# Performance work log

Measured on AMD Instinct MI355X. Metric: run time of the kernel, lower is better.

## Reference

```python
import jax, jax.numpy as jnp
import numpy as np
import math

H = 512       # hidden_dim
NL = 4        # num_layers
N2 = 32       # d_state // 2
B, L = 8, 4096
DT_MIN, DT_MAX = 1e-3, 1e-1
EPS = 1e-5


def _layer_norm(x, gamma, beta):
    mu = jnp.mean(x, axis=-1, keepdims=True)
    var = jnp.mean(jnp.square(x - mu), axis=-1, keepdims=True)
    return (x - mu) * jax.lax.rsqrt(var + EPS) * gamma + beta


def setup_inputs() -> dict:
    key = jax.random.key(0)
    ks = jax.random.split(key, 8)
    x = jax.random.normal(ks[0], (B, L, H), dtype=jnp.float32)
    # S4DKernel buffers / params, stacked over layers
    log_dt = jax.random.uniform(ks[1], (NL, H)) * (math.log(DT_MAX) - math.log(DT_MIN)) + math.log(DT_MIN)
    A_imag = jnp.broadcast_to(math.pi * jnp.arange(N2, dtype=jnp.float32), (NL, H, N2)).copy()
    log_A_real = jnp.full((NL, H, N2), math.log(0.5), dtype=jnp.float32)
    C = jax.random.normal(ks[2], (NL, H, N2, 2), dtype=jnp.float32)  # view_as_real of cfloat
    D = jax.random.normal(ks[3], (NL, H), dtype=jnp.float32)
    # 1x1 Conv1d h -> 2h (pointwise linear over channels)
    W = jax.random.normal(ks[4], (NL, 2 * H, H), dtype=jnp.float32) / math.sqrt(H)
    b = jax.random.normal(ks[5], (NL, 2 * H), dtype=jnp.float32) * 0.01
    gamma = jnp.ones((NL, H), dtype=jnp.float32)
    beta = jnp.zeros((NL, H), dtype=jnp.float32)
    return dict(x=x, log_dt=log_dt, A_imag=A_imag, log_A_real=log_A_real,
                C=C, D=D, W=W, b=b, gamma=gamma, beta=beta)


def reference(x, log_dt, A_imag, log_A_real, C, D, W, b, gamma, beta):
    Bsz, Lseq, h = x.shape
    t = jnp.arange(Lseq, dtype=jnp.float32)
    for i in range(NL):
        # --- S4D kernel generation ---
        dt = jnp.exp(log_dt[i])                                    # (h,)
        Cc = C[i, ..., 0] + 1j * C[i, ..., 1]                      # (h, n)
        A = -jnp.exp(log_A_real[i]) + 1j * A_imag[i]               # (h, n)
        dA = A * dt[:, None]                                       # (h, n)
        Cmod = Cc * (jnp.exp(dA) - 1.0) / A                        # (h, n)
        # Vandermonde: exp(dA * l), reduced over state dim
        K = 2.0 * jnp.einsum('hn,hnl->hl', Cmod,
                             jnp.exp(dA[:, :, None] * t)).real     # (h, L)
        # --- FFT long convolution ---
        u = jnp.transpose(x, (0, 2, 1))                            # (B, h, L)
        kf = jnp.fft.rfft(K, n=2 * Lseq)                           # (h, L+1)
        uf = jnp.fft.rfft(u, n=2 * Lseq)                           # (B, h, L+1)
        y = jnp.fft.irfft(uf * kf, n=2 * Lseq)[..., :Lseq]         # (B, h, L)
        y = y + u * D[i][:, None]
        y = jax.nn.gelu(y, approximate=False)                      # torch nn.GELU default (erf)
        # 1x1 conv h -> 2h then GLU over channel dim
        z = jnp.einsum('oh,bhl->bol', W[i], y) + b[i][None, :, None]
        a, g = jnp.split(z, 2, axis=1)
        y = a * jax.nn.sigmoid(g)                                  # (B, h, L)
        y = jnp.transpose(y, (0, 2, 1))                            # (B, L, h)
        x = _layer_norm(y + x, gamma[i], beta[i])
    return x
```

## Files before the change

kernel.cpp:

```cpp
#include <hip/hip_runtime.h>
#include <hip/hip_bf16.h>
#include <math.h>

#define H 512
#define NL 4
#define N2 32
#define Bsz 8
#define Lseq 4096
#define BT (Bsz*Lseq)
#define LC2 64
#define NCC (BT/LC2)
#define CPB (Lseq/LC2)

typedef __attribute__((ext_vector_type(8))) short short8;
typedef __attribute__((ext_vector_type(4))) float float4v;


__device__ __forceinline__ float bf2f(unsigned short u) {
    union { unsigned int i; float f; } x; x.i = ((unsigned int)u) << 16; return x.f;
}
__device__ __forceinline__ unsigned short f2bf(float f) {
    union { float f; unsigned int i; } x; x.f = f;
    unsigned int u = x.i + 0x7fff + ((x.i >> 16) & 1);
    return (unsigned short)(u >> 16);
}
__device__ __forceinline__ uint2 pack4bf(float a, float b, float c, float d) {
    uint2 r;
    r.x = (unsigned)f2bf(a) | ((unsigned)f2bf(b) << 16);
    r.y = (unsigned)f2bf(c) | ((unsigned)f2bf(d) << 16);
    return r;
}
__device__ __forceinline__ void async_copy16(const void* g, void* l) {
    __builtin_amdgcn_global_load_lds(
        (const __attribute__((address_space(1))) void*)g,
        (__attribute__((address_space(3))) void*)l, 16, 0, 0);
}

__global__ void wconv_kernel(const float* __restrict__ W, unsigned short* __restrict__ Wbf) {
    int tid = blockIdx.x * 256 + threadIdx.x;
    Wbf[tid] = f2bf(W[tid]);
}

__global__ void params_kernel(const float* __restrict__ log_dt, const float* __restrict__ A_imag,
                              const float* __restrict__ log_A_real, const float* __restrict__ Cin,
                              float* __restrict__ dA, float* __restrict__ Ct) {
    int tid = blockIdx.x * 256 + threadIdx.x;
    int h = tid % H;
    int n = (tid / H) % N2;
    int layer = tid / (H * N2);
    float dt = expf(log_dt[layer * H + h]);
    int pidx = (layer * H + h) * N2 + n;
    float Are = -expf(log_A_real[pidx]);
    float Aim = A_imag[pidx];
    float dre = Are * dt, dim = Aim * dt;
    float er = expf(dre);
    float lre = er * cosf(dim), lim = er * sinf(dim);
    float nre = lre - 1.0f, nim = lim;
    float inv = 1.0f / (Are * Are + Aim * Aim);
    float tre = (nre * Are + nim * Aim) * inv;
    float tim = (nim * Are - nre * Aim) * inv;
    float Ccre = Cin[pidx * 2], Ccim = Cin[pidx * 2 + 1];
    int oidx = ((layer * N2 + n) * 2) * H + h;
    dA[oidx] = dre;  dA[oidx + H] = dim;
    Ct[oidx] = 2.0f * (Ccre * tre - Ccim * tim);
    Ct[oidx + H] = 2.0f * (Ccre * tim + Ccim * tre);
}

__global__ void kergen_k_kernel(const float* __restrict__ dA, const float* __restrict__ Ct,
                                unsigned short* __restrict__ kmat) {
    int t = blockIdx.x * 256 + threadIdx.x;
    int d = t & 63;
    int h = (t >> 6) & (H - 1);
    int layer = t >> 15;
    float fd = (float)d;
    float sum = 0.f;
    for (int n = 0; n < N2; n++) {
        int base = ((layer * N2 + n) * 2) * H + h;
        float dre = dA[base], dim = dA[base + H];
        float Ctr = Ct[base], Cti = Ct[base + H];
        float e = expf(dre * fd);
        sum += Ctr * e * cosf(dim * fd) - Cti * e * sinf(dim * fd);
    }
    kmat[t] = f2bf(sum);
}

__global__ void kergenW_kernel(const float* __restrict__ dA, unsigned short* __restrict__ Wst, int layer) {
    int t = blockIdx.x * 256 + threadIdx.x;
    int j = t & 63;
    int r = (t >> 6) & 63;
    int h = t >> 12;
    int n = r >> 1;
    int base = ((layer * N2 + n) * 2) * H + h;
    float dre = dA[base], dim = dA[base + H];
    float p = (float)(63 - j);
    float e = expf(dre * p);
    Wst[t] = f2bf((r & 1) ? e * sinf(dim * p) : e * cosf(dim * p));
}

__global__ void kergenV_kernel(const float* __restrict__ dA, const float* __restrict__ Ct,
                               unsigned short* __restrict__ Vl, int layer) {
    int t = blockIdx.x * 256 + threadIdx.x;
    int c2 = t & 63;
    int l = (t >> 6) & 63;
    int h = t >> 12;
    int n = c2 >> 1;
    int base = ((layer * N2 + n) * 2) * H + h;
    float dre = dA[base], dim = dA[base + H];
    float Ctr = Ct[base], Cti = Ct[base + H];
    float q = (float)(l + 1);
    float e = expf(dre * q);
    float ar = e * cosf(dim * q), ai = e * sinf(dim * q);
    float vre = Ctr * ar - Cti * ai;
    float vim = Ctr * ai + Cti * ar;
    Vl[t] = f2bf((c2 & 1) ? -vim : vre);
}

__global__ __launch_bounds__(256) void t1_f32_kernel(const float* __restrict__ xi,
                                                     unsigned short* __restrict__ ut) {
    __shared__ float tile[64][68];
    int bx = blockIdx.x;
    int pt = bx & 511, ht = bx >> 9;
    int p0 = pt * 64, h0 = ht * 64;
    int t = threadIdx.x;
    int jr = t & 15, ib = t >> 4;
#pragma unroll
    for (int pass = 0; pass < 4; pass++) {
        int i = ib + pass * 16;
        float4 v = *(const float4*)(xi + (size_t)(p0 + i) * H + h0 + jr * 4);
        tile[i][jr * 4 + 0] = v.x; tile[i][jr * 4 + 1] = v.y;
        tile[i][jr * 4 + 2] = v.z; tile[i][jr * 4 + 3] = v.w;
    }
    __syncthreads();
#pragma unroll
    for (int pass = 0; pass < 4; pass++) {
        int i2 = ib + pass * 16;
        int j2 = jr * 4;
        uint2 pk = pack4bf(tile[j2][i2], tile[j2 + 1][i2], tile[j2 + 2][i2], tile[j2 + 3][i2]);
        *(uint2*)(ut + (size_t)(h0 + i2) * BT + p0 + j2) = pk;
    }
}

__global__ __launch_bounds__(256) void t1_bf16_kernel(const unsigned short* __restrict__ xi,
                                                      unsigned short* __restrict__ ut) {
    __shared__ unsigned short tile[64][72];
    int bx = blockIdx.x;
    int pt = bx & 511, ht = bx >> 9;
    int p0 = pt * 64, h0 = ht * 64;
    int t = threadIdx.x;
    int jr = t & 7, ib = t >> 3;
#pragma unroll
    for (int pass = 0; pass < 2; pass++) {
        int i = ib + pass * 32;
        short8 v = *reinterpret_cast<const short8*>(xi + (size_t)(p0 + i) * H + h0 + jr * 8);
#pragma unroll
        for (int e = 0; e < 8; e++) tile[i][jr * 8 + e] = (unsigned short)v[e];
    }
    __syncthreads();
    int hr = t >> 2, bg = t & 3;
    short8 o0, o1;
#pragma unroll
    for (int r = 0; r < 8; r++) o0[r] = (short)tile[bg * 16 + r][hr];
#pragma unroll
    for (int r = 0; r < 8; r++) o1[r] = (short)tile[bg * 16 + 8 + r][hr];
    unsigned short* dst = ut + (size_t)(h0 + hr) * BT + p0 + bg * 16;
    *reinterpret_cast<short8*>(dst) = o0;
    *reinterpret_cast<short8*>(dst + 8) = o1;
}

__global__ __launch_bounds__(256) void states_kernel(const unsigned short* __restrict__ ut,
                                                     const unsigned short* __restrict__ Wst,
                                                     unsigned short* __restrict__ Sloc) {
    int h = blockIdx.x;
    int wave = threadIdx.x >> 6, lane = threadIdx.x & 63;
    int r16 = lane & 15, quad = lane >> 4;
    const unsigned short* uh = ut + (size_t)h * BT;
    const unsigned short* wh = Wst + (size_t)h * 64 * 64;
    unsigned short* sh = Sloc + (size_t)h * NCC * 64;
    for (int nt = 0; nt < 8; nt++) {
        int cc0 = wave * 128 + nt * 16;
        float4v acc[4] = {};
#pragma unroll
        for (int k0 = 0; k0 < 64; k0 += 32) {
            short8 bf = *reinterpret_cast<const short8*>(uh + (size_t)(cc0 + r16) * 64 + k0 + quad * 8);
#pragma unroll
            for (int mt = 0; mt < 4; mt++) {
                short8 af = *reinterpret_cast<const short8*>(wh + (mt * 16 + r16) * 64 + k0 + quad * 8);
                acc[mt] = __builtin_amdgcn_mfma_f32_16x16x32_bf16(af, bf, acc[mt], 0, 0, 0);
            }
        }
        int cc = cc0 + r16;
#pragma unroll
        for (int mt = 0; mt < 4; mt++) {
            uint2 pk = pack4bf(acc[mt][0], acc[mt][1], acc[mt][2], acc[mt][3]);
            *(uint2*)(sh + (size_t)cc * 64 + mt * 16 + quad * 4) = pk;
        }
    }
}

__global__ void combine_kernel(unsigned short* __restrict__ Sloc, const float* __restrict__ dA, int layer) {
    int t = blockIdx.x * 256 + threadIdx.x;
    int n = t & 31;
    int b = (t >> 5) & 7;
    int h = t >> 8;
    int base = ((layer * N2 + n) * 2) * H + h;
    float dre = dA[base], dim = dA[base + H];
    float e = expf(dre * 64.f);
    float Lr = e * cosf(dim * 64.f), Li = e * sinf(dim * 64.f);
    unsigned int* p = (unsigned int*)Sloc + ((size_t)h * NCC + b * CPB) * 32 + n;
    float sr = 0.f, si = 0.f;
    for (int c = 0; c < CPB; c++) {
        unsigned int v = p[(size_t)c * 32];
        float pr = bf2f(v & 0xffff), pi = bf2f(v >> 16);
        p[(size_t)c * 32] = (unsigned)f2bf(sr) | ((unsigned)f2bf(si) << 16);
        float nr = fmaf(Lr, sr, fmaf(-Li, si, pr));
        float ni = fmaf(Lr, si, fmaf(Li, sr, pi));
        sr = nr; si = ni;
    }
}

__global__ __launch_bounds__(256) void conv_kernel(const unsigned short* __restrict__ ut,
                                                   const unsigned short* __restrict__ kmat,
                                                   const unsigned short* __restrict__ Vl,
                                                   const unsigned short* __restrict__ Sent,
                                                   const float* __restrict__ Dp,
                                                   unsigned short* __restrict__ yt, int layer) {
    __shared__ unsigned short T[64][72];
    int h = blockIdx.x, half = blockIdx.y;
    int t = threadIdx.x;
    const unsigned short* km = kmat + ((size_t)layer * H + h) * 64;
    {
        int l = t >> 2, j0 = (t & 3) * 16;
#pragma unroll
        for (int g = 0; g < 2; g++) {
            short8 v;
#pragma unroll
            for (int e = 0; e < 8; e++) {
                int j = j0 + g * 8 + e;
                v[e] = (j <= l) ? (short)km[l - j] : (short)0;
            }
            *reinterpret_cast<short8*>(&T[l][j0 + g * 8]) = v;
        }
    }
    __syncthreads();
    int wave = t >> 6, lane = t & 63;
    int r16 = lane & 15, quad = lane >> 4;
    const unsigned short* uh = ut + (size_t)h * BT;
    const unsigned short* vh = Vl + (size_t)h * 64 * 64;
    const unsigned short* eh = Sent + (size_t)h * NCC * 64;
    unsigned short* yh = yt + (size_t)h * BT;
    float Dh = Dp[layer * H + h];
    for (int nt = 0; nt < 4; nt++) {
        int cc0 = half * 256 + wave * 64 + nt * 16;
        float4v acc[4] = {};
#pragma unroll
        for (int k0 = 0; k0 < 64; k0 += 32) {
            short8 bf = *reinterpret_cast<const short8*>(uh + (size_t)(cc0 + r16) * 64 + k0 + quad * 8);
#pragma unroll
            for (int mt = 0; mt < 4; mt++) {
                short8 af = *reinterpret_cast<const short8*>(&T[mt * 16 + r16][k0 + quad * 8]);
                acc[mt] = __builtin_amdgcn_mfma_f32_16x16x32_bf16(af, bf, acc[mt], 0, 0, 0);
            }
        }
#pragma unroll
        for (int k0 = 0; k0 < 64; k0 += 32) {
            short8 bf = *reinterpret_cast<const short8*>(eh + (size_t)(cc0 + r16) * 64 + k0 + quad * 8);
#pragma unroll
            for (int mt = 0; mt < 4; mt++) {
                short8 af = *reinterpret_cast<const short8*>(vh + (mt * 16 + r16) * 64 + k0 + quad * 8);
                acc[mt] = __builtin_amdgcn_mfma_f32_16x16x32_bf16(af, bf, acc[mt], 0, 0, 0);
            }
        }
        int cc = cc0 + r16;
#pragma unroll
        for (int mt = 0; mt < 4; mt++) {
            size_t p = (size_t)cc * 64 + mt * 16 + quad * 4;
            ushort4 uu = *(const ushort4*)(uh + p);
            float o[4];
#pragma unroll
            for (int r = 0; r < 4; r++) {
                float y = acc[mt][r] + Dh * bf2f(((const unsigned short*)&uu)[r]);
                o[r] = 0.5f * y * (1.0f + erff(y * 0.70710678118654752f));
            }
            *(uint2*)(yh + p) = pack4bf(o[0], o[1], o[2], o[3]);
        }
    }
}

__global__ __launch_bounds__(256) void transpose2_kernel(const unsigned short* __restrict__ yt,
                                                         unsigned short* __restrict__ yb) {
    __shared__ unsigned short tile[64][72];
    int bx = blockIdx.x;
    int pt = bx & 511, ht = bx >> 9;
    int p0 = pt * 64, h0 = ht * 64;
    int t = threadIdx.x;
    int jr = t & 7, ib = t >> 3;
#pragma unroll
    for (int pass = 0; pass < 2; pass++) {
        int i = ib + pass * 32;
        short8 v = *reinterpret_cast<const short8*>(yt + (size_t)(h0 + i) * BT + p0 + jr * 8);
#pragma unroll
        for (int e = 0; e < 8; e++) tile[i][jr * 8 + e] = (unsigned short)v[e];
    }
    __syncthreads();
    int pp = t >> 2, hg = t & 3;
    short8 o0, o1;
#pragma unroll
    for (int r = 0; r < 8; r++) o0[r] = (short)tile[hg * 16 + r][pp];
#pragma unroll
    for (int r = 0; r < 8; r++) o1[r] = (short)tile[hg * 16 + 8 + r][pp];
    unsigned short* dst = yb + (size_t)(p0 + pp) * H + h0 + hg * 16;
    *reinterpret_cast<short8*>(dst) = o0;
    *reinterpret_cast<short8*>(dst + 8) = o1;
}

__global__ __launch_bounds__(256) void gemm_glu_kernel(const unsigned short* __restrict__ ybf,
                                                       const unsigned short* __restrict__ Wbf,
                                                       const float* __restrict__ bias,
                                                       unsigned short* __restrict__ yo, int layer) {
    __shared__ unsigned short As[3][128 * 32];
    __shared__ unsigned short Bs[3][128 * 32];
    int tid = threadIdx.x;
    int wave = tid >> 6, lane = tid & 63;
    int wr = wave >> 1, wc = wave & 1;
    int r16 = lane & 15, quad = lane >> 4;
    int m0 = blockIdx.x * 128;
    int o0 = blockIdx.y * 64;
    const unsigned short* Wl = Wbf + (size_t)layer * 2 * H * H;

    int srow = lane >> 2;
    int scol = ((lane & 3) ^ ((srow >> 1) & 3)) * 8;
    const unsigned short* aS0 = ybf + ((size_t)(m0 + wave * 16 + srow)) * H + scol;
    const unsigned short* aS1 = aS0 + (size_t)64 * H;
    const unsigned short* bSA = Wl + ((size_t)(o0 + wave * 16 + srow)) * H + scol;
    const unsigned short* bSG = bSA + (size_t)512 * H;
    const int aoff0 = (wave * 16) * 32;
    const int aoff1 = (64 + wave * 16) * 32;

    int rcol = (quad ^ ((r16 >> 1) & 3)) * 8;

    float4v acc_a[4][2] = {}, acc_g[4][2] = {};

    async_copy16(aS0,      &As[0][aoff0]);
    async_copy16(aS1,      &As[0][aoff1]);
    async_copy16(bSA,      &Bs[0][aoff0]);
    async_copy16(bSG,      &Bs[0][aoff1]);
    async_copy16(aS0 + 32, &As[1][aoff0]);
    async_copy16(aS1 + 32, &As[1][aoff1]);
    async_copy16(bSA + 32, &Bs[1][aoff0]);
    async_copy16(bSG + 32, &Bs[1][aoff1]);
    asm volatile("s_waitcnt vmcnt(4)" ::: "memory");
    __builtin_amdgcn_s_barrier();

#pragma unroll
    for (int ks = 0; ks < 16; ++ks) {
        const int b = ks % 3;
        if (ks < 14) {
            const int nb = (ks + 2) % 3;
            const int kn = (ks + 2) * 32;
            async_copy16(aS0 + kn, &As[nb][aoff0]);
            async_copy16(aS1 + kn, &As[nb][aoff1]);
            async_copy16(bSA + kn, &Bs[nb][aoff0]);
            async_copy16(bSG + kn, &Bs[nb][aoff1]);
        }

        short8 af[4], ba[2], bg[2];
#pragma unroll
        for (int mi = 0; mi < 4; mi++)
            af[mi] = *reinterpret_cast<const short8*>(&As[b][(wr * 64 + mi * 16 + r16) * 32 + rcol]);
#pragma unroll
        for (int ni = 0; ni < 2; ni++) {
            ba[ni] = *reinterpret_cast<const short8*>(&Bs[b][(wc * 32 + ni * 16 + r16) * 32 + rcol]);
            bg[ni] = *reinterpret_cast<const short8*>(&Bs[b][(64 + wc * 32 + ni * 16 + r16) * 32 + rcol]);
        }
#pragma unroll
        for (int mi = 0; mi < 4; mi++)
#pragma unroll
            for (int ni = 0; ni < 2; ni++) {
                acc_a[mi][ni] = __builtin_amdgcn_mfma_f32_16x16x32_bf16(af[mi], ba[ni], acc_a[mi][ni], 0, 0, 0);
                acc_g[mi][ni] = __builtin_amdgcn_mfma_f32_16x16x32_bf16(af[mi], bg[ni], acc_g[mi][ni], 0, 0, 0);
            }

        if (ks < 14) {
            asm volatile("s_waitcnt vmcnt(4) lgkmcnt(0)" ::: "memory");
            __builtin_amdgcn_s_barrier();
        } else if (ks == 14) {
            asm volatile("s_waitcnt vmcnt(0) lgkmcnt(0)" ::: "memory");
            __builtin_amdgcn_s_barrier();
        }
    }

    const float* bl = bias + layer * 2 * H;
#pragma unroll
    for (int ni = 0; ni < 2; ni++) {
        int o = o0 + wc * 32 + ni * 16 + r16;
        float ba_ = bl[o], bg_ = bl[H + o];
#pragma unroll
        for (int mi = 0; mi < 4; mi++)
#pragma unroll
            for (int r = 0; r < 4; r++) {
                int l = m0 + wr * 64 + mi * 16 + quad * 4 + r;
                float av = acc_a[mi][ni][r] + ba_;
                float gv = acc_g[mi][ni][r] + bg_;
                yo[(size_t)l * H + o] = f2bf(av * (1.0f / (1.0f + expf(-gv))));
            }
    }
}

__global__ __launch_bounds__(256) void ln_kernel(const unsigned short* __restrict__ yo,
                                                 const float* __restrict__ xf,
                                                 const unsigned short* __restrict__ xb,
                                                 const float* __restrict__ gamma, const float* __restrict__ beta,
                                                 float* __restrict__ of, unsigned short* __restrict__ ob,
                                                 int in_f32, int out_f32, int layer) {
    int wave = threadIdx.x >> 6, lane = threadIdx.x & 63;
    size_t row = (size_t)blockIdx.x * 4 + wave;
    const unsigned short* yp = yo + row * H + lane * 8;
    short8 yv = *reinterpret_cast<const short8*>(yp);
    float v[8];
    if (in_f32) {
        const float* xp = xf + row * H + lane * 8;
        float4 x0 = *(const float4*)(xp);
        float4 x1 = *(const float4*)(xp + 4);
        v[0] = bf2f((unsigned short)yv[0]) + x0.x; v[1] = bf2f((unsigned short)yv[1]) + x0.y;
        v[2] = bf2f((unsigned short)yv[2]) + x0.z; v[3] = bf2f((unsigned short)yv[3]) + x0.w;
        v[4] = bf2f((unsigned short)yv[4]) + x1.x; v[5] = bf2f((unsigned short)yv[5]) + x1.y;
        v[6] = bf2f((unsigned short)yv[6]) + x1.z; v[7] = bf2f((unsigned short)yv[7]) + x1.w;
    } else {
        const unsigned short* xp = xb + row * H + lane * 8;
        short8 xv = *reinterpret_cast<const short8*>(xp);
#pragma unroll
        for (int i = 0; i < 8; i++)
            v[i] = bf2f((unsigned short)yv[i]) + bf2f((unsigned short)xv[i]);
    }
    float s = 0.f, s2 = 0.f;
#pragma unroll
    for (int i = 0; i < 8; i++) { s += v[i]; s2 = fmaf(v[i], v[i], s2); }
#pragma unroll
    for (int off = 32; off; off >>= 1) {
        s += __shfl_xor(s, off);
        s2 += __shfl_xor(s2, off);
    }
    float mu = s * (1.0f / H);
    float var = s2 * (1.0f / H) - mu * mu;
    float inv = rsqrtf(var + 1e-5f);
    const float* gl = gamma + layer * H + lane * 8;
    const float* bl = beta + layer * H + lane * 8;
    float o[8];
#pragma unroll
    for (int i = 0; i < 8; i++)
        o[i] = (v[i] - mu) * inv * gl[i] + bl[i];
    if (out_f32) {
        float* op = of + row * H + lane * 8;
        *(float4*)(op) = make_float4(o[0], o[1], o[2], o[3]);
        *(float4*)(op + 4) = make_float4(o[4], o[5], o[6], o[7]);
    } else {
        unsigned short* op = ob + row * H + lane * 8;
        uint2 p0 = pack4bf(o[0], o[1], o[2], o[3]);
        uint2 p1 = pack4bf(o[4], o[5], o[6], o[7]);
        *(uint2*)(op) = p0;
        *(uint2*)(op + 4) = p1;
    }
}

extern "C" void kernel_launch(void* const* d_in, const int* in_sizes, int n_in,
                              void* d_out, int out_size, void* d_ws, size_t ws_size,
                              hipStream_t stream) {
    const float* x          = (const float*)d_in[0];
    const float* log_dt     = (const float*)d_in[1];
    const float* A_imag     = (const float*)d_in[2];
    const float* log_A_real = (const float*)d_in[3];
    const float* C          = (const float*)d_in[4];
    const float* D          = (const float*)d_in[5];
    const float* W          = (const float*)d_in[6];
    const float* bias       = (const float*)d_in[7];
    const float* gamma      = (const float*)d_in[8];
    const float* beta       = (const float*)d_in[9];

    char* ws = (char*)d_ws;
    unsigned short* xR   = (unsigned short*)(ws + 0);
    unsigned short* Sloc = (unsigned short*)(ws + 67108864);
    unsigned short* u_t  = (unsigned short*)(ws + 100663296);
    unsigned short* ybf  = (unsigned short*)(ws + 100663296);
    unsigned short* y_t  = (unsigned short*)(ws + 134217728);
    unsigned short* yo   = (unsigned short*)(ws + 134217728);
    unsigned short* Wbf  = (unsigned short*)(ws + 167772160);
    unsigned short* WV   = (unsigned short*)(ws + 171966464);
    unsigned short* kmat = (unsigned short*)(ws + 176160768);
    float*          dA   = (float*)(ws + 176422912);
    float*          Ct   = (float*)(ws + 176947200);
    float* xout_final    = (float*)d_out;

    wconv_kernel<<<NL * 2 * H * H / 256, 256, 0, stream>>>(W, Wbf);
    params_kernel<<<NL * N2 * H / 256, 256, 0, stream>>>(log_dt, A_imag, log_A_real, C, dA, Ct);
    kergen_k_kernel<<<NL * H * 64 / 256, 256, 0, stream>>>(dA, Ct, kmat);

    for (int layer = 0; layer < NL; ++layer) {
        if (layer == 0)
            t1_f32_kernel<<<4096, 256, 0, stream>>>(x, u_t);
        else
            t1_bf16_kernel<<<4096, 256, 0, stream>>>(xR, u_t);
        kergenW_kernel<<<H * 64 * 64 / 256, 256, 0, stream>>>(dA, WV, layer);
        states_kernel<<<H, 256, 0, stream>>>(u_t, WV, Sloc);
        combine_kernel<<<H * Bsz * N2 / 256, 256, 0, stream>>>(Sloc, dA, layer);
        kergenV_kernel<<<H * 64 * 64 / 256, 256, 0, stream>>>(dA, Ct, WV, layer);
        conv_kernel<<<dim3(H, 2), 256, 0, stream>>>(u_t, kmat, WV, Sloc, D, y_t, layer);
        transpose2_kernel<<<4096, 256, 0, stream>>>(y_t, ybf);
        gemm_glu_kernel<<<dim3(BT / 128, H / 64), 256, 0, stream>>>(ybf, Wbf, bias, yo, layer);
        int in_f32 = (layer == 0), out_f32 = (layer == NL - 1);
        ln_kernel<<<BT / 4, 256, 0, stream>>>(yo, x, xR, gamma, beta,
                                              xout_final, xR, in_f32, out_f32, layer);
    }
}
```

Before: 854.8 us.

## Load GEMM weight fragments directly from global into registers, bypassing LDS

In the GEMM+GLU kernel, the weight operand no longer goes through a triple-buffered LDS tile. Each wave now loads its W fragments straight from global memory into registers with dwordx4 loads, double-buffered across k-steps. The aim is to cut LDS footprint and LDS read traffic and free shared memory for occupancy. In exchange, the waves sharing a column duplicate their global weight loads, and each iteration's wait now also covers those register loads, which may expose global latency.

```diff
diff --git a/kernel.cpp b/kernel.cpp
--- a/kernel.cpp
+++ b/kernel.cpp
@@ -34,6 +34,9 @@
     __builtin_amdgcn_global_load_lds(
         (const __attribute__((address_space(1))) void*)g,
         (__attribute__((address_space(3))) void*)l, 16, 0, 0);
+}
+__device__ __forceinline__ void gload16(short8* d, const unsigned short* p) {
+    asm volatile("global_load_dwordx4 %0, %1, off" : "=v"(*d) : "v"(p) : "memory");
 }
 
 __global__ void wconv_kernel(const float* __restrict__ W, unsigned short* __restrict__ Wbf) {
@@ -318,7 +321,6 @@
                                                        const float* __restrict__ bias,
                                                        unsigned short* __restrict__ yo, int layer) {
     __shared__ unsigned short As[3][128 * 32];
-    __shared__ unsigned short Bs[3][128 * 32];
     int tid = threadIdx.x;
     int wave = tid >> 6, lane = tid & 63;
     int wr = wave >> 1, wc = wave & 1;
@@ -331,60 +333,69 @@
     int scol = ((lane & 3) ^ ((srow >> 1) & 3)) * 8;
     const unsigned short* aS0 = ybf + ((size_t)(m0 + wave * 16 + srow)) * H + scol;
     const unsigned short* aS1 = aS0 + (size_t)64 * H;
-    const unsigned short* bSA = Wl + ((size_t)(o0 + wave * 16 + srow)) * H + scol;
-    const unsigned short* bSG = bSA + (size_t)512 * H;
     const int aoff0 = (wave * 16) * 32;
     const int aoff1 = (64 + wave * 16) * 32;
 
     int rcol = (quad ^ ((r16 >> 1) & 3)) * 8;
 
+    const unsigned short* wA0 = Wl + (size_t)(o0 + wc * 32 +  0 + r16) * H + quad * 8;
+    const unsigned short* wA1 = Wl + (size_t)(o0 + wc * 32 + 16 + r16) * H + quad * 8;
+    const unsigned short* wG0 = wA0 + (size_t)512 * H;
+    const unsigned short* wG1 = wA1 + (size_t)512 * H;
+
+    short8 wa0[2], wa1[2], wg0[2], wg1[2];
+
     float4v acc_a[4][2] = {}, acc_g[4][2] = {};
 
-    async_copy16(aS0,      &As[0][aoff0]);
-    async_copy16(aS1,      &As[0][aoff1]);
-    async_copy16(bSA,      &Bs[0][aoff0]);
-    async_copy16(bSG,      &Bs[0][aoff1]);
+    async_copy16(aS0, &As[0][aoff0]);
+    async_copy16(aS1, &As[0][aoff1]);
+    gload16(&wa0[0], wA0);
+    gload16(&wa1[0], wA1);
+    gload16(&wg0[0], wG0);
+    gload16(&wg1[0], wG1);
     async_copy16(aS0 + 32, &As[1][aoff0]);
     async_copy16(aS1 + 32, &As[1][aoff1]);
-    async_copy16(bSA + 32, &Bs[1][aoff0]);
-    async_copy16(bSG + 32, &Bs[1][aoff1]);
-    asm volatile("s_waitcnt vmcnt(4)" ::: "memory");
+    asm volatile("s_waitcnt vmcnt(2)" ::: "memory");
+    __builtin_amdgcn_sched_barrier(0);
     __builtin_amdgcn_s_barrier();
 
 #pragma unroll
     for (int ks = 0; ks < 16; ++ks) {
         const int b = ks % 3;
+        const int cur = ks & 1, nxt = (ks + 1) & 1;
+        if (ks < 15) {
+            const int kw = (ks + 1) * 32;
+            gload16(&wa0[nxt], wA0 + kw);
+            gload16(&wa1[nxt], wA1 + kw);
+            gload16(&wg0[nxt], wG0 + kw);
+            gload16(&wg1[nxt], wG1 + kw);
+        }
         if (ks < 14) {
             const int nb = (ks + 2) % 3;
             const int kn = (ks + 2) * 32;
             async_copy16(aS0 + kn, &As[nb][aoff0]);
             async_copy16(aS1 + kn, &As[nb][aoff1]);
-            async_copy16(bSA + kn, &Bs[nb][aoff0]);
-            async_copy16(bSG + kn, &Bs[nb][aoff1]);
-        }
-
-        short8 af[4], ba[2], bg[2];
+        }
+
+        short8 af[4];
 #pragma unroll
         for (int mi = 0; mi < 4; mi++)
             af[mi] = *reinterpret_cast<const short8*>(&As[b][(wr * 64 + mi * 16 + r16) * 32 + rcol]);
 #pragma unroll
-        for (int ni = 0; ni < 2; ni++) {
-            ba[ni] = *reinterpret_cast<const short8*>(&Bs[b][(wc * 32 + ni * 16 + r16) * 32 + rcol]);
-            bg[ni] = *reinterpret_cast<const short8*>(&Bs[b][(64 + wc * 32 + ni * 16 + r16) * 32 + rcol]);
-        }
-#pragma unroll
-        for (int mi = 0; mi < 4; mi++)
-#pragma unroll
-            for (int ni = 0; ni < 2; ni++) {
-                acc_a[mi][ni] = __builtin_amdgcn_mfma_f32_16x16x32_bf16(af[mi], ba[ni], acc_a[mi][ni], 0, 0, 0);
-                acc_g[mi][ni] = __builtin_amdgcn_mfma_f32_16x16x32_bf16(af[mi], bg[ni], acc_g[mi][ni], 0, 0, 0);
-            }
+        for (int mi = 0; mi < 4; mi++) {
+            acc_a[mi][0] = __builtin_amdgcn_mfma_f32_16x16x32_bf16(af[mi], wa0[cur], acc_a[mi][0], 0, 0, 0);
+            acc_a[mi][1] = __builtin_amdgcn_mfma_f32_16x16x32_bf16(af[mi], wa1[cur], acc_a[mi][1], 0, 0, 0);
+            acc_g[mi][0] = __builtin_amdgcn_mfma_f32_16x16x32_bf16(af[mi], wg0[cur], acc_g[mi][0], 0, 0, 0);
+            acc_g[mi][1] = __builtin_amdgcn_mfma_f32_16x16x32_bf16(af[mi], wg1[cur], acc_g[mi][1], 0, 0, 0);
+        }
 
         if (ks < 14) {
-            asm volatile("s_waitcnt vmcnt(4) lgkmcnt(0)" ::: "memory");
+            asm volatile("s_waitcnt vmcnt(2) lgkmcnt(0)" ::: "memory");
+            __builtin_amdgcn_sched_barrier(0);
             __builtin_amdgcn_s_barrier();
         } else if (ks == 14) {
             asm volatile("s_waitcnt vmcnt(0) lgkmcnt(0)" ::: "memory");
+            __builtin_amdgcn_sched_barrier(0);
             __builtin_amdgcn_s_barrier();
         }
     }
```

Result: slower. 955.8 us (+11.8%).

## Fuse layernorm with next-layer input transpose and vectorize LDS tile stores

Applied to the files above, without the earlier changes.

A new ln_t kernel computes the residual add and layernorm for 64 rows per block and writes the bf16 row-major activations. It also transposes the normalized tile through shared memory straight into the channel-major u_t buffer. That removes the separate t1_bf16 transpose pass and its extra global read of xR for layers 1-3. The two transpose kernels also store their loaded vectors to LDS with one wide store instead of element-wise writes. The trade-off is a heavier kernel: 64 floats per thread, about 66KB of LDS per block and only 512 blocks, which may limit occupancy.

```diff
diff --git a/kernel.cpp b/kernel.cpp
--- a/kernel.cpp
+++ b/kernel.cpp
@@ -127,8 +127,7 @@
     for (int pass = 0; pass < 4; pass++) {
         int i = ib + pass * 16;
         float4 v = *(const float4*)(xi + (size_t)(p0 + i) * H + h0 + jr * 4);
-        tile[i][jr * 4 + 0] = v.x; tile[i][jr * 4 + 1] = v.y;
-        tile[i][jr * 4 + 2] = v.z; tile[i][jr * 4 + 3] = v.w;
+        *(float4*)(&tile[i][jr * 4]) = v;
     }
     __syncthreads();
 #pragma unroll
@@ -138,33 +137,6 @@
         uint2 pk = pack4bf(tile[j2][i2], tile[j2 + 1][i2], tile[j2 + 2][i2], tile[j2 + 3][i2]);
         *(uint2*)(ut + (size_t)(h0 + i2) * BT + p0 + j2) = pk;
     }
-}
-
-__global__ __launch_bounds__(256) void t1_bf16_kernel(const unsigned short* __restrict__ xi,
-                                                      unsigned short* __restrict__ ut) {
-    __shared__ unsigned short tile[64][72];
-    int bx = blockIdx.x;
-    int pt = bx & 511, ht = bx >> 9;
-    int p0 = pt * 64, h0 = ht * 64;
-    int t = threadIdx.x;
-    int jr = t & 7, ib = t >> 3;
-#pragma unroll
-    for (int pass = 0; pass < 2; pass++) {
-        int i = ib + pass * 32;
-        short8 v = *reinterpret_cast<const short8*>(xi + (size_t)(p0 + i) * H + h0 + jr * 8);
-#pragma unroll
-        for (int e = 0; e < 8; e++) tile[i][jr * 8 + e] = (unsigned short)v[e];
-    }
-    __syncthreads();
-    int hr = t >> 2, bg = t & 3;
-    short8 o0, o1;
-#pragma unroll
-    for (int r = 0; r < 8; r++) o0[r] = (short)tile[bg * 16 + r][hr];
-#pragma unroll
-    for (int r = 0; r < 8; r++) o1[r] = (short)tile[bg * 16 + 8 + r][hr];
-    unsigned short* dst = ut + (size_t)(h0 + hr) * BT + p0 + bg * 16;
-    *reinterpret_cast<short8*>(dst) = o0;
-    *reinterpret_cast<short8*>(dst + 8) = o1;
 }
 
 __global__ __launch_bounds__(256) void states_kernel(const unsigned short* __restrict__ ut,
@@ -298,8 +270,7 @@
     for (int pass = 0; pass < 2; pass++) {
         int i = ib + pass * 32;
         short8 v = *reinterpret_cast<const short8*>(yt + (size_t)(h0 + i) * BT + p0 + jr * 8);
-#pragma unroll
-        for (int e = 0; e < 8; e++) tile[i][jr * 8 + e] = (unsigned short)v[e];
+        *reinterpret_cast<short8*>(&tile[i][jr * 8]) = v;
     }
     __syncthreads();
     int pp = t >> 2, hg = t & 3;
@@ -403,6 +374,92 @@
                 float gv = acc_g[mi][ni][r] + bg_;
                 yo[(size_t)l * H + o] = f2bf(av * (1.0f / (1.0f + expf(-gv))));
             }
+    }
+}
+
+__global__ __launch_bounds__(256) void ln_t_kernel(const unsigned short* __restrict__ yo,
+                                                   const float* __restrict__ xf,
+                                                   const unsigned short* __restrict__ xb,
+                                                   const float* __restrict__ gamma,
+                                                   const float* __restrict__ beta,
+                                                   unsigned short* __restrict__ xR,
+                                                   unsigned short* __restrict__ ut,
+                                                   int in_f32, int layer) {
+    __shared__ unsigned short tl[64][520];
+    int t = threadIdx.x;
+    int p0 = blockIdx.x * 64;
+    int lane8 = t & 7;
+    int rowb = t >> 3;
+    const float* gl = gamma + layer * H;
+    const float* bl = beta + layer * H;
+#pragma unroll
+    for (int rr = 0; rr < 2; rr++) {
+        int row = rowb + rr * 32;
+        size_t gbase = (size_t)(p0 + row) * H;
+        float v[64];
+        float s = 0.f, s2 = 0.f;
+#pragma unroll
+        for (int cc = 0; cc < 8; cc++) {
+            int h0 = (lane8 + cc * 8) * 8;
+            short8 yv = *reinterpret_cast<const short8*>(yo + gbase + h0);
+            if (in_f32) {
+                float4 x0 = *(const float4*)(xf + gbase + h0);
+                float4 x1 = *(const float4*)(xf + gbase + h0 + 4);
+                v[cc * 8 + 0] = bf2f((unsigned short)yv[0]) + x0.x;
+                v[cc * 8 + 1] = bf2f((unsigned short)yv[1]) + x0.y;
+                v[cc * 8 + 2] = bf2f((unsigned short)yv[2]) + x0.z;
+                v[cc * 8 + 3] = bf2f((unsigned short)yv[3]) + x0.w;
+                v[cc * 8 + 4] = bf2f((unsigned short)yv[4]) + x1.x;
+                v[cc * 8 + 5] = bf2f((unsigned short)yv[5]) + x1.y;
+                v[cc * 8 + 6] = bf2f((unsigned short)yv[6]) + x1.z;
+                v[cc * 8 + 7] = bf2f((unsigned short)yv[7]) + x1.w;
+            } else {
+                short8 xv = *reinterpret_cast<const short8*>(xb + gbase + h0);
+#pragma unroll
+                for (int i = 0; i < 8; i++)
+                    v[cc * 8 + i] = bf2f((unsigned short)yv[i]) + bf2f((unsigned short)xv[i]);
+            }
+#pragma unroll
+            for (int i = 0; i < 8; i++) { s += v[cc * 8 + i]; s2 = fmaf(v[cc * 8 + i], v[cc * 8 + i], s2); }
+        }
+        s += __shfl_xor(s, 1);  s2 += __shfl_xor(s2, 1);
+        s += __shfl_xor(s, 2);  s2 += __shfl_xor(s2, 2);
+        s += __shfl_xor(s, 4);  s2 += __shfl_xor(s2, 4);
+        float mu = s * (1.0f / H);
+        float var = s2 * (1.0f / H) - mu * mu;
+        float inv = rsqrtf(var + 1e-5f);
+#pragma unroll
+        for (int cc = 0; cc < 8; cc++) {
+            int h0 = (lane8 + cc * 8) * 8;
+            float4 g0 = *(const float4*)(gl + h0);
+            float4 g1 = *(const float4*)(gl + h0 + 4);
+            float4 b0 = *(const float4*)(bl + h0);
+            float4 b1 = *(const float4*)(bl + h0 + 4);
+            short8 pk;
+            pk[0] = (short)f2bf((v[cc * 8 + 0] - mu) * inv * g0.x + b0.x);
+            pk[1] = (short)f2bf((v[cc * 8 + 1] - mu) * inv * g0.y + b0.y);
+            pk[2] = (short)f2bf((v[cc * 8 + 2] - mu) * inv * g0.z + b0.z);
+            pk[3] = (short)f2bf((v[cc * 8 + 3] - mu) * inv * g0.w + b0.w);
+            pk[4] = (short)f2bf((v[cc * 8 + 4] - mu) * inv * g1.x + b1.x);
+            pk[5] = (short)f2bf((v[cc * 8 + 5] - mu) * inv * g1.y + b1.y);
+            pk[6] = (short)f2bf((v[cc * 8 + 6] - mu) * inv * g1.z + b1.z);
+            pk[7] = (short)f2bf((v[cc * 8 + 7] - mu) * inv * g1.w + b1.w);
+            *reinterpret_cast<short8*>(xR + gbase + h0) = pk;
+            *reinterpret_cast<short8*>(&tl[row][h0]) = pk;
+        }
+    }
+    __syncthreads();
+#pragma unroll
+    for (int hh = 0; hh < 2; hh++) {
+        int h = t + hh * 256;
+        unsigned short* dst = ut + (size_t)h * BT + p0;
+#pragma unroll
+        for (int pc = 0; pc < 8; pc++) {
+            short8 o;
+#pragma unroll
+            for (int e = 0; e < 8; e++) o[e] = (short)tl[pc * 8 + e][h];
+            *reinterpret_cast<short8*>(dst + pc * 8) = o;
+        }
     }
 }
 
@@ -497,8 +554,6 @@
     for (int layer = 0; layer < NL; ++layer) {
         if (layer == 0)
             t1_f32_kernel<<<4096, 256, 0, stream>>>(x, u_t);
-        else
-            t1_bf16_kernel<<<4096, 256, 0, stream>>>(xR, u_t);
         kergenW_kernel<<<H * 64 * 64 / 256, 256, 0, stream>>>(dA, WV, layer);
         states_kernel<<<H, 256, 0, stream>>>(u_t, WV, Sloc);
         combine_kernel<<<H * Bsz * N2 / 256, 256, 0, stream>>>(Sloc, dA, layer);
@@ -506,8 +561,12 @@
         conv_kernel<<<dim3(H, 2), 256, 0, stream>>>(u_t, kmat, WV, Sloc, D, y_t, layer);
         transpose2_kernel<<<4096, 256, 0, stream>>>(y_t, ybf);
         gemm_glu_kernel<<<dim3(BT / 128, H / 64), 256, 0, stream>>>(ybf, Wbf, bias, yo, layer);
-        int in_f32 = (layer == 0), out_f32 = (layer == NL - 1);
-        ln_kernel<<<BT / 4, 256, 0, stream>>>(yo, x, xR, gamma, beta,
-                                              xout_final, xR, in_f32, out_f32, layer);
-    }
-}
+        if (layer < NL - 1) {
+            ln_t_kernel<<<BT / 64, 256, 0, stream>>>(yo, x, xR, gamma, beta,
+                                                     xR, u_t, (layer == 0) ? 1 : 0, layer);
+        } else {
+            ln_kernel<<<BT / 4, 256, 0, stream>>>(yo, x, xR, gamma, beta,
+                                                  xout_final, xR, 0, 1, layer);
+        }
+    }
+}
```

Measured after the change: 854.3 us. About the same (-0.1%).
